# Performance work log

Hardware: AMD Instinct MI355X
Metric: run time of the kernel (lower is better)

## Reference

```python
import jax, jax.numpy as jnp
import numpy as np

GROUPS = 32
EPS = 1e-5


def group_norm(x, weight, bias):
    # x: [B, C, H, W]; normalize per (group, H, W) as torch nn.GroupNorm
    B, C, H, W = x.shape
    xg = x.reshape(B, GROUPS, C // GROUPS, H, W)
    mean = xg.mean(axis=(2, 3, 4), keepdims=True)
    var = xg.var(axis=(2, 3, 4), keepdims=True)
    xg = (xg - mean) * jax.lax.rsqrt(var + EPS)
    x = xg.reshape(B, C, H, W)
    return x * weight[None, :, None, None] + bias[None, :, None, None]


def setup_inputs() -> dict:
    key = jax.random.key(0)
    ks = jax.random.split(key, 8)
    B, C, H, W = 2, 512, 64, 64
    s = 1.0 / np.sqrt(C)  # linear-init-like scale to keep logits sane
    return {
        "x": jax.random.normal(ks[0], (B, C, H, W), dtype=jnp.float32),
        "gn_weight": jnp.ones((C,), jnp.float32),
        "gn_bias": jnp.zeros((C,), jnp.float32),
        "wq": jax.random.normal(ks[1], (C, C), jnp.float32) * s,
        "bq": jnp.zeros((C,), jnp.float32),
        "wk": jax.random.normal(ks[2], (C, C), jnp.float32) * s,
        "bk": jnp.zeros((C,), jnp.float32),
        "wv": jax.random.normal(ks[3], (C, C), jnp.float32) * s,
        "bv": jnp.zeros((C,), jnp.float32),
        "wo": jax.random.normal(ks[4], (C, C), jnp.float32) * s,
        "bo": jnp.zeros((C,), jnp.float32),
    }


def reference(x, gn_weight, gn_bias, wq, bq, wk, bk, wv, bv, wo, bo):
    B, C, H, W = x.shape
    residual = x
    h = group_norm(x, gn_weight, gn_bias)
    # [B, N, C] tokens, N = H*W
    t = h.reshape(B, C, H * W).transpose(0, 2, 1)
    q = t @ wq.T + bq
    k = t @ wk.T + bk
    v = t @ wv.T + bv
    scale = C ** (-0.5)
    # naive full attention: [B, N, N]
    attn = jax.nn.softmax(jnp.einsum("bnc,bmc->bnm", q, k) * scale, axis=-1)
    out = jnp.einsum("bnm,bmc->bnc", attn, v)
    out = out @ wo.T + bo
    out = out.transpose(0, 2, 1).reshape(B, C, H, W)
    return out + residual
```

## Files before the change

kernel.cpp:

```cpp
#include <hip/hip_runtime.h>
#include <cstddef>
#include <cstdint>


typedef __attribute__((ext_vector_type(8))) short frag8;
typedef __attribute__((ext_vector_type(4))) float f32x4;

#define GLOAD16(g, l)                                                        \
    __builtin_amdgcn_global_load_lds(                                        \
        (const __attribute__((address_space(1))) void*)(g),                  \
        (__attribute__((address_space(3))) void*)(l), 16, 0, 0)

__device__ __forceinline__ float b2f(unsigned short u) {
    union { unsigned u32; float f; } v; v.u32 = ((unsigned)u) << 16; return v.f;
}
__device__ __forceinline__ unsigned short f2bu(float f) {
    unsigned u = __float_as_uint(f);
    unsigned r = u + 0x7fffu + ((u >> 16) & 1u);
    return (unsigned short)(r >> 16);
}

__global__ __launch_bounds__(256) void cast_f32_bf16(const float* __restrict__ src,
                                                     unsigned short* __restrict__ dst,
                                                     int n) {
    int i = (blockIdx.x * 256 + threadIdx.x) * 8;
    if (i >= n) return;
    float4 a = *reinterpret_cast<const float4*>(src + i);
    float4 b = *reinterpret_cast<const float4*>(src + i + 4);
    float vv[8] = {a.x, a.y, a.z, a.w, b.x, b.y, b.z, b.w};
    union { unsigned short u16[8]; uint4 v; } o;
#pragma unroll
    for (int j = 0; j < 8; ++j) o.u16[j] = f2bu(vv[j]);
    *reinterpret_cast<uint4*>(dst + i) = o.v;
}

__global__ __launch_bounds__(256) void gn_stats(const float* __restrict__ x,
                                                float* __restrict__ stats) {
    const int tid = threadIdx.x;
    const float* p = x + (size_t)blockIdx.x * 65536;
    float s = 0.f, ss = 0.f;
    for (int i = tid * 8; i < 65536; i += 2048) {
        float4 a = *reinterpret_cast<const float4*>(p + i);
        float4 b = *reinterpret_cast<const float4*>(p + i + 4);
        float vv[8] = {a.x, a.y, a.z, a.w, b.x, b.y, b.z, b.w};
#pragma unroll
        for (int j = 0; j < 8; ++j) { s += vv[j]; ss += vv[j] * vv[j]; }
    }
#pragma unroll
    for (int o = 32; o; o >>= 1) { s += __shfl_xor(s, o, 64); ss += __shfl_xor(ss, o, 64); }
    __shared__ float rs[4], rss[4];
    int wv = tid >> 6, lane = tid & 63;
    if (lane == 0) { rs[wv] = s; rss[wv] = ss; }
    __syncthreads();
    if (tid == 0) {
        float S1 = rs[0] + rs[1] + rs[2] + rs[3];
        float S2 = rss[0] + rss[1] + rss[2] + rss[3];
        float mean = S1 * (1.f / 65536.f);
        float var  = fmaxf(S2 * (1.f / 65536.f) - mean * mean, 0.f);
        stats[blockIdx.x * 2 + 0] = mean;
        stats[blockIdx.x * 2 + 1] = rsqrtf(var + 1e-5f);
    }
}

__global__ __launch_bounds__(256) void prep_all(const float* __restrict__ x,
                                                float* __restrict__ stats,
                                                const float* __restrict__ wq,
                                                const float* __restrict__ wk,
                                                const float* __restrict__ wv,
                                                const float* __restrict__ wo,
                                                const float* __restrict__ bq,
                                                const float* __restrict__ bk,
                                                const float* __restrict__ bv,
                                                const float* __restrict__ bo,
                                                unsigned short* __restrict__ wB0,
                                                unsigned short* __restrict__ wB3,
                                                unsigned short* __restrict__ bB0,
                                                unsigned short* __restrict__ bB3) {
    const int tid = threadIdx.x;
    const int bx = blockIdx.x;
    if (bx < 64) {
        const float* p = x + (size_t)bx * 65536;
        float s = 0.f, ss = 0.f;
        for (int i = tid * 8; i < 65536; i += 2048) {
            float4 a = *reinterpret_cast<const float4*>(p + i);
            float4 b = *reinterpret_cast<const float4*>(p + i + 4);
            float vv[8] = {a.x, a.y, a.z, a.w, b.x, b.y, b.z, b.w};
#pragma unroll
            for (int j = 0; j < 8; ++j) { s += vv[j]; ss += vv[j] * vv[j]; }
        }
#pragma unroll
        for (int o = 32; o; o >>= 1) { s += __shfl_xor(s, o, 64); ss += __shfl_xor(ss, o, 64); }
        __shared__ float rs[4], rss[4];
        int wvi = tid >> 6, lane = tid & 63;
        if (lane == 0) { rs[wvi] = s; rss[wvi] = ss; }
        __syncthreads();
        if (tid == 0) {
            float S1 = rs[0] + rs[1] + rs[2] + rs[3];
            float S2 = rss[0] + rss[1] + rss[2] + rss[3];
            float mean = S1 * (1.f / 65536.f);
            float var  = fmaxf(S2 * (1.f / 65536.f) - mean * mean, 0.f);
            stats[bx * 2 + 0] = mean;
            stats[bx * 2 + 1] = rsqrtf(var + 1e-5f);
        }
    } else if (bx < 576) {
        const int j = bx - 64;
        const int w = j >> 7;
        const int b128 = j & 127;
        const float* src = (w == 0) ? wq : (w == 1) ? wk : (w == 2) ? wv : wo;
        unsigned short* dst = (w == 0) ? wB0 : (w == 1) ? wB0 + 262144
                              : (w == 2) ? wB0 + 524288 : wB3;
        int i = (b128 * 256 + tid) * 8;
        float4 a = *reinterpret_cast<const float4*>(src + i);
        float4 b = *reinterpret_cast<const float4*>(src + i + 4);
        float vv[8] = {a.x, a.y, a.z, a.w, b.x, b.y, b.z, b.w};
        union { unsigned short u16[8]; uint4 v; } o;
#pragma unroll
        for (int jj = 0; jj < 8; ++jj) o.u16[jj] = f2bu(vv[jj]);
        *reinterpret_cast<uint4*>(dst + i) = o.v;
    } else {
        const int j = bx - 576;
        const float* src = (j == 0) ? bq : (j == 1) ? bk : (j == 2) ? bv : bo;
        unsigned short* dst = (j == 0) ? bB0 : (j == 1) ? bB0 + 512
                              : (j == 2) ? bB0 + 1024 : bB3;
        int i = tid * 8;
        if (i < 512) {
            float4 a = *reinterpret_cast<const float4*>(src + i);
            float4 b = *reinterpret_cast<const float4*>(src + i + 4);
            float vv[8] = {a.x, a.y, a.z, a.w, b.x, b.y, b.z, b.w};
            union { unsigned short u16[8]; uint4 v; } o;
#pragma unroll
            for (int jj = 0; jj < 8; ++jj) o.u16[jj] = f2bu(vv[jj]);
            *reinterpret_cast<uint4*>(dst + i) = o.v;
        }
    }
}

__global__ __launch_bounds__(256) void build_t(const float* __restrict__ x,
                                               const float* __restrict__ stats,
                                               const float* __restrict__ gnw,
                                               const float* __restrict__ gnb,
                                               unsigned short* __restrict__ t) {
    __shared__ unsigned short tile[64 * 66];
    const int b = blockIdx.z, c0 = blockIdx.y * 64, hw0 = blockIdx.x * 64;
#pragma unroll
    for (int it = 0; it < 2; ++it) {
        int idx = it * 256 + threadIdx.x;
        int c = idx >> 3, v8 = idx & 7;
        int cg = c0 + c;
        int g = cg >> 4;
        float mean = stats[(b * 32 + g) * 2 + 0];
        float rstd = stats[(b * 32 + g) * 2 + 1];
        float sc = rstd * gnw[cg];
        float sh = gnb[cg] - mean * sc;
        const float* src = x + ((size_t)(b * 512 + cg)) * 4096 + hw0 + v8 * 8;
        float4 a = *reinterpret_cast<const float4*>(src);
        float4 bb = *reinterpret_cast<const float4*>(src + 4);
        float vv[8] = {a.x, a.y, a.z, a.w, bb.x, bb.y, bb.z, bb.w};
#pragma unroll
        for (int j = 0; j < 8; ++j)
            tile[c * 66 + v8 * 8 + j] = f2bu(vv[j] * sc + sh);
    }
    __syncthreads();
#pragma unroll
    for (int it = 0; it < 2; ++it) {
        int idx = it * 256 + threadIdx.x;
        int hw = idx >> 3, v8 = idx & 7;
        union { unsigned short u16[8]; uint4 v; } outv;
#pragma unroll
        for (int j = 0; j < 8; ++j) outv.u16[j] = tile[(v8 * 8 + j) * 66 + hw];
        *reinterpret_cast<uint4*>(t + ((size_t)(b * 4096 + hw0 + hw)) * 512 + c0 + v8 * 8) =
            outv.v;
    }
}

template <int MODE>
__global__ __launch_bounds__(256) void gemm_bt(const unsigned short* __restrict__ A,
                                               const unsigned short* __restrict__ B,
                                               const unsigned short* __restrict__ bias,
                                               const float* __restrict__ resid,
                                               unsigned short* __restrict__ C,
                                               float* __restrict__ Cf,
                                               int M, int N, int K, float alpha,
                                               size_t zA, size_t zB, size_t zC) {
    __shared__ __attribute__((aligned(16))) unsigned short As[128 * 32];
    __shared__ __attribute__((aligned(16))) unsigned short Bs[128 * 32];

    A += (size_t)blockIdx.z * zA;
    B += (size_t)blockIdx.z * zB;
    C += (size_t)blockIdx.z * zC;

    const int tid = threadIdx.x;
    const int lane = tid & 63, wv = tid >> 6;
    const int lrow = lane & 15, quad = lane >> 4;
    const int wr = (wv & 1) * 64, wc = (wv >> 1) * 64;

    const unsigned short* Ag = A + ((size_t)blockIdx.x * 128 + wv * 16 + (lane >> 2)) * K + (lane & 3) * 8;
    const unsigned short* Bg = B + ((size_t)blockIdx.y * 128 + wv * 16 + (lane >> 2)) * K + (lane & 3) * 8;
    unsigned short* Asw = As + wv * 512;
    unsigned short* Bsw = Bs + wv * 512;
    const size_t rowskip = (size_t)64 * K;

    f32x4 acc[4][4] = {};

    for (int k0 = 0; k0 < K; k0 += 32) {
        GLOAD16(Ag + k0,           Asw);
        GLOAD16(Ag + k0 + rowskip, Asw + 2048);
        GLOAD16(Bg + k0,           Bsw);
        GLOAD16(Bg + k0 + rowskip, Bsw + 2048);
        __syncthreads();

        frag8 af[4], bf[4];
        const unsigned short* ap = As + (wr + lrow) * 32 + quad * 8;
        const unsigned short* bp = Bs + (wc + lrow) * 32 + quad * 8;
#pragma unroll
        for (int i = 0; i < 4; ++i) af[i] = *reinterpret_cast<const frag8*>(ap + i * 512);
#pragma unroll
        for (int j = 0; j < 4; ++j) bf[j] = *reinterpret_cast<const frag8*>(bp + j * 512);
#pragma unroll
        for (int i = 0; i < 4; ++i)
#pragma unroll
            for (int j = 0; j < 4; ++j)
                acc[i][j] = __builtin_amdgcn_mfma_f32_16x16x32_bf16(af[i], bf[j], acc[i][j], 0, 0, 0);
        __syncthreads();
    }

    const int rowBase = blockIdx.x * 128 + wr + quad * 4;
    const int colBase = blockIdx.y * 128 + wc + lrow;
#pragma unroll
    for (int j = 0; j < 4; ++j) {
        const int col = colBase + j * 16;
        float badd = 0.f;
        if (MODE == 3 && bias) badd = b2f(bias[col]);
#pragma unroll
        for (int i = 0; i < 4; ++i) {
            const int row = rowBase + i * 16;
#pragma unroll
            for (int r = 0; r < 4; ++r) {
                const int rr = row + r;
                float v = acc[i][j][r];
                if (MODE == 2) v *= alpha;
                v += badd;
                if (MODE == 2) {
                    C[(size_t)rr * N + col] = f2bu(v);
                } else {
                    size_t addr = ((size_t)(rr >> 12) * 512 + col) * 4096 + (rr & 4095);
                    Cf[addr] = v + resid[addr];
                }
            }
        }
    }
}

__global__ __launch_bounds__(256) void gemm_qkv(const unsigned short* __restrict__ A,
                                                const unsigned short* __restrict__ Ball,
                                                const unsigned short* __restrict__ biasAll,
                                                unsigned short* __restrict__ q,
                                                unsigned short* __restrict__ k,
                                                unsigned short* __restrict__ vT) {
    __shared__ __attribute__((aligned(16))) unsigned short As[128 * 32];
    __shared__ __attribute__((aligned(16))) unsigned short Bs[128 * 32];
    const int K = 512;

    const int tid = threadIdx.x;
    const int lane = tid & 63, wv = tid >> 6;
    const int lrow = lane & 15, quad = lane >> 4;
    const int wr = (wv & 1) * 64, wc = (wv >> 1) * 64;

    const unsigned short* B = Ball + (size_t)blockIdx.y * 128 * 512;
    const unsigned short* Ag = A + ((size_t)blockIdx.x * 128 + wv * 16 + (lane >> 2)) * K + (lane & 3) * 8;
    const unsigned short* Bg = B + ((size_t)(wv * 16 + (lane >> 2))) * K + (lane & 3) * 8;
    unsigned short* Asw = As + wv * 512;
    unsigned short* Bsw = Bs + wv * 512;
    const size_t rowskip = (size_t)64 * K;

    f32x4 acc[4][4] = {};

    for (int k0 = 0; k0 < K; k0 += 32) {
        GLOAD16(Ag + k0,           Asw);
        GLOAD16(Ag + k0 + rowskip, Asw + 2048);
        GLOAD16(Bg + k0,           Bsw);
        GLOAD16(Bg + k0 + rowskip, Bsw + 2048);
        __syncthreads();

        frag8 af[4], bf[4];
        const unsigned short* ap = As + (wr + lrow) * 32 + quad * 8;
        const unsigned short* bp = Bs + (wc + lrow) * 32 + quad * 8;
#pragma unroll
        for (int i = 0; i < 4; ++i) af[i] = *reinterpret_cast<const frag8*>(ap + i * 512);
#pragma unroll
        for (int j = 0; j < 4; ++j) bf[j] = *reinterpret_cast<const frag8*>(bp + j * 512);
#pragma unroll
        for (int i = 0; i < 4; ++i)
#pragma unroll
            for (int j = 0; j < 4; ++j)
                acc[i][j] = __builtin_amdgcn_mfma_f32_16x16x32_bf16(af[i], bf[j], acc[i][j], 0, 0, 0);
        __syncthreads();
    }

    const int rowBase = blockIdx.x * 128 + wr + quad * 4;
    const int colBase = wc + lrow;
    const int gbase = blockIdx.y * 128;
#pragma unroll
    for (int j = 0; j < 4; ++j) {
        const int colL = colBase + j * 16;
        const int gcol = gbase + colL;
        const float badd = b2f(biasAll[gcol]);
#pragma unroll
        for (int i = 0; i < 4; ++i) {
            const int row = rowBase + i * 16;
#pragma unroll
            for (int r = 0; r < 4; ++r) {
                const int rr = row + r;
                float v = acc[i][j][r] + badd;
                if (blockIdx.y < 4) {
                    q[(size_t)rr * 512 + gcol] = f2bu(v);
                } else if (blockIdx.y < 8) {
                    k[(size_t)rr * 512 + (gcol - 512)] = f2bu(v);
                } else {
                    int ch = gcol - 1024;
                    vT[((size_t)(rr >> 12) * 512 + ch) * 4096 + (rr & 4095)] = f2bu(v);
                }
            }
        }
    }
}

__global__ __launch_bounds__(512, 4) void s_gemm(const unsigned short* __restrict__ qIn,
                                                 const unsigned short* __restrict__ kIn,
                                                 unsigned short* __restrict__ Sout,
                                                 float alpha) {
    __shared__ __attribute__((aligned(16))) unsigned short Ab[2][8192];
    __shared__ __attribute__((aligned(16))) unsigned short Bb[2][8192];

    const int tid = threadIdx.x;
    const int lane = tid & 63, w = tid >> 6;
    const int lrow = lane & 15, quad = lane >> 4;
    const int wm = w & 1, wn = w >> 1;
    const int z = blockIdx.z;

    const unsigned short* A = qIn + (size_t)z * 2097152;
    const unsigned short* B = kIn + (size_t)z * 2097152;
    unsigned short* C = Sout + (size_t)z * 16777216;

    const int srow = w * 8 + (lane >> 3);
    const int skc  = ((lane & 7) ^ (lane >> 3)) * 8;
    const unsigned short* Ag = A + ((size_t)blockIdx.x * 128 + srow) * 512 + skc;
    const unsigned short* Bg = B + ((size_t)blockIdx.y * 128 + srow) * 512 + skc;
    const size_t rowskip64 = (size_t)64 * 512;

    f32x4 acc[4][2] = {};

#define SG_STAGE(cur, kt)                                                    \
    do {                                                                     \
        const unsigned short* a_ = Ag + (size_t)(kt) * 64;                   \
        const unsigned short* b_ = Bg + (size_t)(kt) * 64;                   \
        GLOAD16(a_,             &Ab[cur][w * 512]);                          \
        GLOAD16(a_ + rowskip64, &Ab[cur][4096 + w * 512]);                   \
        GLOAD16(b_,             &Bb[cur][w * 512]);                          \
        GLOAD16(b_ + rowskip64, &Bb[cur][4096 + w * 512]);                   \
    } while (0)

#define SG_COMPUTE(cur)                                                      \
    do {                                                                     \
        const int rbA = (wm * 64 + lrow) * 64;                               \
        const int rbB = (wn * 32 + lrow) * 64;                               \
        _Pragma("unroll")                                                    \
        for (int kk = 0; kk < 2; ++kk) {                                     \
            const int us = (((kk * 4 + quad) ^ (lrow & 7)) * 8);             \
            frag8 af[4], bf[2];                                              \
            _Pragma("unroll")                                                \
            for (int i = 0; i < 4; ++i)                                      \
                af[i] = *reinterpret_cast<const frag8*>(&Ab[cur][rbA + i * 1024 + us]); \
            _Pragma("unroll")                                                \
            for (int j2 = 0; j2 < 2; ++j2)                                   \
                bf[j2] = *reinterpret_cast<const frag8*>(&Bb[cur][rbB + j2 * 1024 + us]); \
            _Pragma("unroll")                                                \
            for (int i = 0; i < 4; ++i)                                      \
                _Pragma("unroll")                                            \
                for (int j2 = 0; j2 < 2; ++j2)                               \
                    acc[i][j2] = __builtin_amdgcn_mfma_f32_16x16x32_bf16(    \
                        af[i], bf[j2], acc[i][j2], 0, 0, 0);                 \
        }                                                                    \
    } while (0)

    SG_STAGE(0, 0);
    asm volatile("s_waitcnt vmcnt(0)" ::: "memory");
    __builtin_amdgcn_s_barrier();
    __builtin_amdgcn_sched_barrier(0);

    int cur = 0;
    for (int kt = 0; kt < 7; ++kt) {
        SG_STAGE(cur ^ 1, kt + 1);
        __builtin_amdgcn_sched_barrier(0);
        SG_COMPUTE(cur);
        asm volatile("s_waitcnt vmcnt(0)" ::: "memory");
        __builtin_amdgcn_s_barrier();
        __builtin_amdgcn_sched_barrier(0);
        cur ^= 1;
    }
    SG_COMPUTE(cur);

#undef SG_STAGE
#undef SG_COMPUTE

    const int rowBase = blockIdx.x * 128 + wm * 64 + quad * 4;
    const int colBase = blockIdx.y * 128 + wn * 32 + lrow;
#pragma unroll
    for (int j2 = 0; j2 < 2; ++j2) {
        const int col = colBase + j2 * 16;
#pragma unroll
        for (int i = 0; i < 4; ++i) {
            const int row = rowBase + i * 16;
#pragma unroll
            for (int r = 0; r < 4; ++r)
                C[(size_t)(row + r) * 4096 + col] = f2bu(acc[i][j2][r] * alpha);
        }
    }
}

__global__ __launch_bounds__(512, 6) void pv_gemm(const unsigned short* __restrict__ S0,
                                                  const unsigned short* __restrict__ vT0,
                                                  unsigned short* __restrict__ O0) {
    __shared__ __attribute__((aligned(16))) unsigned short Ab[2][4096];
    __shared__ __attribute__((aligned(16))) unsigned short Bb[2][8192];

    const int tid = threadIdx.x;
    const int lane = tid & 63, w = tid >> 6;
    const int lrow = lane & 15, quad = lane >> 4;
    const int wm = w & 1, wn = w >> 1;

    const int id = blockIdx.x;
    const int g  = id & 7;
    const int yt = g & 3, z = g >> 2;
    const int xt = id >> 3;

    const unsigned short* A = S0 + (size_t)z * 16777216;
    const unsigned short* B = vT0 + (size_t)z * 2097152;
    unsigned short* C = O0 + (size_t)z * 2097152;

    const int srow = w * 8 + (lane >> 3);
    const int skc  = ((lane & 7) ^ (lane >> 3)) * 8;
    const unsigned short* Ag = A + ((size_t)xt * 64 + srow) * 4096 + skc;
    const unsigned short* Bg = B + ((size_t)(yt * 128 + srow)) * 4096 + skc;
    const size_t rowskip64 = (size_t)64 * 4096;

    f32x4 acc[2][2] = {};

#define PV_STAGE(cur, kt)                                                    \
    do {                                                                     \
        const unsigned short* a_ = Ag + (size_t)(kt) * 64;                   \
        const unsigned short* b_ = Bg + (size_t)(kt) * 64;                   \
        GLOAD16(a_,             &Ab[cur][w * 512]);                          \
        GLOAD16(b_,             &Bb[cur][w * 512]);                          \
        GLOAD16(b_ + rowskip64, &Bb[cur][4096 + w * 512]);                   \
    } while (0)

#define PV_COMPUTE(cur)                                                      \
    do {                                                                     \
        const int rbA = (wm * 32 + lrow) * 64;                               \
        const int rbB = (wn * 32 + lrow) * 64;                               \
        _Pragma("unroll")                                                    \
        for (int kk = 0; kk < 2; ++kk) {                                     \
            const int us = (((kk * 4 + quad) ^ (lrow & 7)) * 8);             \
            frag8 af[2], bf[2];                                              \
            _Pragma("unroll")                                                \
            for (int i = 0; i < 2; ++i)                                      \
                af[i] = *reinterpret_cast<const frag8*>(&Ab[cur][rbA + i * 1024 + us]); \
            _Pragma("unroll")                                                \
            for (int j2 = 0; j2 < 2; ++j2)                                   \
                bf[j2] = *reinterpret_cast<const frag8*>(&Bb[cur][rbB + j2 * 1024 + us]); \
            _Pragma("unroll")                                                \
            for (int i = 0; i < 2; ++i)                                      \
                _Pragma("unroll")                                            \
                for (int j2 = 0; j2 < 2; ++j2)                               \
                    acc[i][j2] = __builtin_amdgcn_mfma_f32_16x16x32_bf16(    \
                        af[i], bf[j2], acc[i][j2], 0, 0, 0);                 \
        }                                                                    \
    } while (0)

    PV_STAGE(0, 0);
    asm volatile("s_waitcnt vmcnt(0)" ::: "memory");
    __builtin_amdgcn_s_barrier();
    __builtin_amdgcn_sched_barrier(0);

    int cur = 0;
    for (int kt = 0; kt < 63; ++kt) {
        PV_STAGE(cur ^ 1, kt + 1);
        __builtin_amdgcn_sched_barrier(0);
        PV_COMPUTE(cur);
        asm volatile("s_waitcnt vmcnt(0)" ::: "memory");
        __builtin_amdgcn_s_barrier();
        __builtin_amdgcn_sched_barrier(0);
        cur ^= 1;
    }
    PV_COMPUTE(cur);

#undef PV_STAGE
#undef PV_COMPUTE

    const int rowBase = xt * 64 + wm * 32 + quad * 4;
    const int colBase = yt * 128 + wn * 32 + lrow;
#pragma unroll
    for (int j2 = 0; j2 < 2; ++j2) {
        const int col = colBase + j2 * 16;
#pragma unroll
        for (int i = 0; i < 2; ++i) {
            const int row = rowBase + i * 16;
#pragma unroll
            for (int r = 0; r < 4; ++r)
                C[(size_t)(row + r) * 512 + col] = f2bu(acc[i][j2][r]);
        }
    }
}

__global__ __launch_bounds__(512, 2) void ksplit_o(const unsigned short* __restrict__ A,
                                                   const unsigned short* __restrict__ B,
                                                   unsigned short* __restrict__ C,
                                                   int N, int K) {
    __shared__ __attribute__((aligned(16))) unsigned char smem[65536];
    const int tid = threadIdx.x;
    const int lane = tid & 63, wv = tid >> 6;
    const int lrow = lane & 15, quad = lane >> 4;
    const int colhalf = wv & 1;
    const int kz = wv >> 1;
    const int Kw = K >> 2;
    const int yt = blockIdx.x;
    const int xt = blockIdx.y;

    unsigned short* Aw = (unsigned short*)smem + wv * 4096;
    unsigned short* Bw = Aw + 2048;

    const unsigned short* Ag = A + ((size_t)xt * 64 + (lane >> 2)) * K + kz * Kw + (lane & 3) * 8;
    const unsigned short* Bg = B + ((size_t)(yt * 128 + colhalf * 64 + (lane >> 2))) * K + kz * Kw + (lane & 3) * 8;
    const size_t rowskip16 = (size_t)16 * K;

    f32x4 acc[4][4] = {};

    for (int k0 = 0; k0 < Kw; k0 += 32) {
        uint4 av[4], bv_[4];
#pragma unroll
        for (int i = 0; i < 4; ++i) {
            av[i]  = *reinterpret_cast<const uint4*>(Ag + k0 + i * rowskip16);
            bv_[i] = *reinterpret_cast<const uint4*>(Bg + k0 + i * rowskip16);
        }
#pragma unroll
        for (int i = 0; i < 4; ++i) {
            *reinterpret_cast<uint4*>(Aw + i * 512 + lane * 8) = av[i];
            *reinterpret_cast<uint4*>(Bw + i * 512 + lane * 8) = bv_[i];
        }
        frag8 af[4], bf[4];
#pragma unroll
        for (int i = 0; i < 4; ++i) {
            af[i] = *reinterpret_cast<const frag8*>(Aw + i * 512 + lrow * 32 + quad * 8);
            bf[i] = *reinterpret_cast<const frag8*>(Bw + i * 512 + lrow * 32 + quad * 8);
        }
        __builtin_amdgcn_s_setprio(1);
#pragma unroll
        for (int i = 0; i < 4; ++i)
#pragma unroll
            for (int j = 0; j < 4; ++j)
                acc[i][j] = __builtin_amdgcn_mfma_f32_16x16x32_bf16(af[i], bf[j], acc[i][j], 0, 0, 0);
        __builtin_amdgcn_s_setprio(0);
    }

    __syncthreads();
    float* fbase = (float*)smem;
    if (kz == 0 || kz == 2) {
        float* f = fbase + (colhalf * 2 + (kz >> 1)) * 4096;
#pragma unroll
        for (int i = 0; i < 4; ++i)
#pragma unroll
            for (int j = 0; j < 4; ++j)
#pragma unroll
                for (int r = 0; r < 4; ++r)
                    f[(i * 16 + quad * 4 + r) * 64 + j * 16 + lrow] = acc[i][j][r];
    }
    __syncthreads();
    if (kz == 1 || kz == 3) {
        float* f = fbase + (colhalf * 2 + (kz >> 1)) * 4096;
#pragma unroll
        for (int i = 0; i < 4; ++i)
#pragma unroll
            for (int j = 0; j < 4; ++j)
#pragma unroll
                for (int r = 0; r < 4; ++r)
                    f[(i * 16 + quad * 4 + r) * 64 + j * 16 + lrow] += acc[i][j][r];
    }
    __syncthreads();
#pragma unroll
    for (int e = 0; e < 16; ++e) {
        int idx = e * 512 + tid;
        int row = idx >> 7, colL = idx & 127;
        int ch = colL >> 6, c = colL & 63;
        float v = fbase[(ch * 2 + 0) * 4096 + row * 64 + c] +
                  fbase[(ch * 2 + 1) * 4096 + row * 64 + c];
        C[((size_t)xt * 64 + row) * N + yt * 128 + colL] = f2bu(v);
    }
}

__global__ __launch_bounds__(256) void softmax_rows(unsigned short* __restrict__ S) {
    __shared__ float red[8];
    const int tid = threadIdx.x;
    const int wv = tid >> 6, lane = tid & 63;
    unsigned short* p = S + (size_t)blockIdx.x * 4096 + tid * 16;

    uint4 r0 = *reinterpret_cast<const uint4*>(p);
    uint4 r1 = *reinterpret_cast<const uint4*>(p + 8);
    unsigned w[8] = {r0.x, r0.y, r0.z, r0.w, r1.x, r1.y, r1.z, r1.w};
    float v[16];
#pragma unroll
    for (int q2 = 0; q2 < 8; ++q2) {
        v[q2 * 2 + 0] = b2f((unsigned short)(w[q2] & 0xffffu));
        v[q2 * 2 + 1] = b2f((unsigned short)(w[q2] >> 16));
    }
    float m = -3.0e38f;
#pragma unroll
    for (int q2 = 0; q2 < 16; ++q2) m = fmaxf(m, v[q2]);
#pragma unroll
    for (int o = 32; o; o >>= 1) m = fmaxf(m, __shfl_xor(m, o, 64));
    if (lane == 0) red[wv] = m;
    __syncthreads();
    m = fmaxf(fmaxf(red[0], red[1]), fmaxf(red[2], red[3]));

    float s = 0.f;
#pragma unroll
    for (int q2 = 0; q2 < 16; ++q2) { v[q2] = __expf(v[q2] - m); s += v[q2]; }
#pragma unroll
    for (int o = 32; o; o >>= 1) s += __shfl_xor(s, o, 64);
    if (lane == 0) red[4 + wv] = s;
    __syncthreads();
    s = red[4] + red[5] + red[6] + red[7];
    const float inv = 1.f / s;

    unsigned ow[8];
#pragma unroll
    for (int q2 = 0; q2 < 8; ++q2) {
        unsigned lo = f2bu(v[q2 * 2 + 0] * inv);
        unsigned hi = f2bu(v[q2 * 2 + 1] * inv);
        ow[q2] = lo | (hi << 16);
    }
    uint4 o0 = {ow[0], ow[1], ow[2], ow[3]};
    uint4 o1 = {ow[4], ow[5], ow[6], ow[7]};
    *reinterpret_cast<uint4*>(p) = o0;
    *reinterpret_cast<uint4*>(p + 8) = o1;
}

__global__ void write_sentinel_f32(float* out, float code) {
    if (threadIdx.x == 0) out[0] = code;
}

extern "C" void kernel_launch(void* const* d_in, const int* in_sizes, int n_in,
                              void* d_out, int out_size, void* d_ws, size_t ws_size,
                              hipStream_t stream) {
    const float* x   = (const float*)d_in[0];
    const float* gnw = (const float*)d_in[1];
    const float* gnb = (const float*)d_in[2];
    const float* wq  = (const float*)d_in[3];
    const float* bq  = (const float*)d_in[4];
    const float* wk  = (const float*)d_in[5];
    const float* bk  = (const float*)d_in[6];
    const float* wv  = (const float*)d_in[7];
    const float* bv  = (const float*)d_in[8];
    const float* wo  = (const float*)d_in[9];
    const float* bo  = (const float*)d_in[10];
    float* out = (float*)d_out;

    bool shapes_ok = (n_in == 11 && in_sizes[0] == 4194304 && in_sizes[1] == 512 &&
                      in_sizes[3] == 262144 && out_size == 4194304);
    size_t half = ws_size / 2;
    if (!shapes_ok || half < (size_t)17831936 + 128 * 4096) {
        write_sentinel_f32<<<1, 64, 0, stream>>>(out, shapes_ok ? 8000.f : 9000.f);
        return;
    }

    unsigned short* ws = (unsigned short*)d_ws;
    unsigned short* t  = ws;
    unsigned short* q  = ws + 4194304;
    unsigned short* k  = ws + 8388608;
    unsigned short* vT = ws + 12582912;
    unsigned short* o  = t;
    const float scale = 0.044194173824159216f;

    unsigned short* wB0 = ws + 16777216;
    unsigned short* bB0 = ws + 17825792;
    float* stats = (float*)(ws + 17827840);

    if (half >= (size_t)50594816) {
        unsigned short* S   = ws + 16777216;
        unsigned short* wB3 = ws + 50331648;
        unsigned short* bB3 = ws + 50593792;
        prep_all<<<580, 256, 0, stream>>>(x, stats, wq, wk, wv, wo, bq, bk, bv, bo,
                                          wB0, wB3, bB0, bB3);
        build_t<<<dim3(64, 8, 2), 256, 0, stream>>>(x, stats, gnw, gnb, t);
        gemm_qkv<<<dim3(64, 12), 256, 0, stream>>>(t, wB0, bB0, q, k, vT);
        s_gemm<<<dim3(32, 32, 2), 512, 0, stream>>>(q, k, S, scale);
        softmax_rows<<<8192, 256, 0, stream>>>(S);
        pv_gemm<<<512, 512, 0, stream>>>(S, vT, o);
        gemm_bt<3><<<dim3(64, 4), 256, 0, stream>>>(o, wB3, bB3, x, nullptr, out,
                                                    8192, 512, 512, 1.f, 0, 0, 0);
        return;
    }

    unsigned short* wB3 = ws + 17563648;
    unsigned short* bB3 = ws + 17827328;

    cast_f32_bf16<<<128, 256, 0, stream>>>(wq, wB0,          262144);
    cast_f32_bf16<<<128, 256, 0, stream>>>(wk, wB0 + 262144, 262144);
    cast_f32_bf16<<<128, 256, 0, stream>>>(wv, wB0 + 524288, 262144);
    cast_f32_bf16<<<1, 256, 0, stream>>>(bq, bB0,        512);
    cast_f32_bf16<<<1, 256, 0, stream>>>(bk, bB0 + 512,  512);
    cast_f32_bf16<<<1, 256, 0, stream>>>(bv, bB0 + 1024, 512);

    gn_stats<<<64, 256, 0, stream>>>(x, stats);
    build_t<<<dim3(64, 8, 2), 256, 0, stream>>>(x, stats, gnw, gnb, t);
    gemm_qkv<<<dim3(64, 12), 256, 0, stream>>>(t, wB0, bB0, q, k, vT);

    if (half >= (size_t)50331648) {
        unsigned short* S = ws + 16777216;
        s_gemm<<<dim3(32, 32, 2), 512, 0, stream>>>(q, k, S, scale);
        softmax_rows<<<8192, 256, 0, stream>>>(S);
        pv_gemm<<<512, 512, 0, stream>>>(S, vT, o);
    } else if (half >= (size_t)33554432) {
        unsigned short* S = ws + 16777216;
        for (int b = 0; b < 2; ++b) {
            const unsigned short* qb  = q  + (size_t)b * 2097152;
            const unsigned short* kb  = k  + (size_t)b * 2097152;
            const unsigned short* vTb = vT + (size_t)b * 2097152;
            unsigned short*       ob  = o  + (size_t)b * 2097152;
            gemm_bt<2><<<dim3(32, 32), 256, 0, stream>>>(qb, kb, nullptr, nullptr, S, nullptr,
                                                         4096, 4096, 512, scale, 0, 0, 0);
            softmax_rows<<<4096, 256, 0, stream>>>(S);
            ksplit_o<<<dim3(4, 64), 512, 0, stream>>>(S, vTb, ob, 512, 4096);
        }
    } else {
        unsigned short* S = ws + 17831936;
        size_t avail = half - 17831936;
        int R = 4096;
        while (R > 128 && (size_t)R * 4096 > avail) R >>= 1;
        for (int b = 0; b < 2; ++b) {
            const unsigned short* qb  = q  + (size_t)b * 2097152;
            const unsigned short* kb  = k  + (size_t)b * 2097152;
            const unsigned short* vTb = vT + (size_t)b * 2097152;
            unsigned short*       ob  = o  + (size_t)b * 2097152;
            for (int r0 = 0; r0 < 4096; r0 += R) {
                gemm_bt<2><<<dim3(R / 128, 32), 256, 0, stream>>>(
                    qb + (size_t)r0 * 512, kb, nullptr, nullptr, S, nullptr, R, 4096, 512, scale,
                    0, 0, 0);
                softmax_rows<<<R, 256, 0, stream>>>(S);
                ksplit_o<<<dim3(4, R / 64), 512, 0, stream>>>(
                    S, vTb, ob + (size_t)r0 * 512, 512, 4096);
            }
        }
    }
    cast_f32_bf16<<<128, 256, 0, stream>>>(wo, wB3, 262144);
    cast_f32_bf16<<<1, 256, 0, stream>>>(bo, bB3, 512);
    gemm_bt<3><<<dim3(64, 4), 256, 0, stream>>>(o, wB3, bB3, x, nullptr, out,
                                                8192, 512, 512, 1.f, 0, 0, 0);
}
```

Measured before the change: 264.5 us.

## Fuse softmax normalization into PV GEMM using precomputed row max and sum

Replaces the in-place softmax pass with a kernel that only computes each row's max and inverse sum of exponentials. The PV GEMM then exponentiates and normalizes the score fragments as it loads them. This removes the write-back of the full score matrix. In exchange, the exponentials are recomputed in every column tile of the GEMM, adding VALU work to its inner loop, and the path needs a slightly larger workspace.

Measured after the change: 347.3 us. 31.3% more time.

```diff
diff --git a/kernel.cpp b/kernel.cpp
--- a/kernel.cpp
+++ b/kernel.cpp
@@ -418,9 +418,50 @@
     }
 }
 
+__global__ __launch_bounds__(256) void row_stats(const unsigned short* __restrict__ S,
+                                                 float* __restrict__ rstat) {
+    __shared__ float red[8];
+    const int tid = threadIdx.x;
+    const int wv = tid >> 6, lane = tid & 63;
+    const unsigned short* p = S + (size_t)blockIdx.x * 4096 + tid * 16;
+
+    uint4 r0 = *reinterpret_cast<const uint4*>(p);
+    uint4 r1 = *reinterpret_cast<const uint4*>(p + 8);
+    unsigned w[8] = {r0.x, r0.y, r0.z, r0.w, r1.x, r1.y, r1.z, r1.w};
+    float v[16];
+#pragma unroll
+    for (int q2 = 0; q2 < 8; ++q2) {
+        v[q2 * 2 + 0] = b2f((unsigned short)(w[q2] & 0xffffu));
+        v[q2 * 2 + 1] = b2f((unsigned short)(w[q2] >> 16));
+    }
+    float m = -3.0e38f;
+#pragma unroll
+    for (int q2 = 0; q2 < 16; ++q2) m = fmaxf(m, v[q2]);
+#pragma unroll
+    for (int o = 32; o; o >>= 1) m = fmaxf(m, __shfl_xor(m, o, 64));
+    if (lane == 0) red[wv] = m;
+    __syncthreads();
+    m = fmaxf(fmaxf(red[0], red[1]), fmaxf(red[2], red[3]));
+
+    float s = 0.f;
+#pragma unroll
+    for (int q2 = 0; q2 < 16; ++q2) s += __expf(v[q2] - m);
+#pragma unroll
+    for (int o = 32; o; o >>= 1) s += __shfl_xor(s, o, 64);
+    if (lane == 0) red[4 + wv] = s;
+    __syncthreads();
+    if (tid == 0) {
+        s = red[4] + red[5] + red[6] + red[7];
+        rstat[blockIdx.x * 2 + 0] = m;
+        rstat[blockIdx.x * 2 + 1] = 1.f / s;
+    }
+}
+
+template <int FUSED>
 __global__ __launch_bounds__(512, 6) void pv_gemm(const unsigned short* __restrict__ S0,
                                                   const unsigned short* __restrict__ vT0,
-                                                  unsigned short* __restrict__ O0) {
+                                                  unsigned short* __restrict__ O0,
+                                                  const float* __restrict__ rstat) {
     __shared__ __attribute__((aligned(16))) unsigned short Ab[2][4096];
     __shared__ __attribute__((aligned(16))) unsigned short Bb[2][8192];
 
@@ -437,6 +478,15 @@
     const unsigned short* A = S0 + (size_t)z * 16777216;
     const unsigned short* B = vT0 + (size_t)z * 2097152;
     unsigned short* C = O0 + (size_t)z * 2097152;
+
+    float mrow[2] = {0.f, 0.f}, irow[2] = {1.f, 1.f};
+    if (FUSED) {
+        const int grow = z * 4096 + xt * 64 + wm * 32 + lrow;
+        mrow[0] = rstat[(size_t)grow * 2 + 0];
+        irow[0] = rstat[(size_t)grow * 2 + 1];
+        mrow[1] = rstat[(size_t)(grow + 16) * 2 + 0];
+        irow[1] = rstat[(size_t)(grow + 16) * 2 + 1];
+    }
 
     const int srow = w * 8 + (lane >> 3);
     const int skc  = ((lane & 7) ^ (lane >> 3)) * 8;
@@ -466,6 +516,18 @@
             _Pragma("unroll")                                                \
             for (int i = 0; i < 2; ++i)                                      \
                 af[i] = *reinterpret_cast<const frag8*>(&Ab[cur][rbA + i * 1024 + us]); \
+            if (FUSED) {                                                     \
+                _Pragma("unroll")                                            \
+                for (int i = 0; i < 2; ++i) {                                \
+                    frag8 a = af[i], r;                                      \
+                    _Pragma("unroll")                                        \
+                    for (int e = 0; e < 8; ++e) {                            \
+                        float f = b2f((unsigned short)a[e]);                 \
+                        r[e] = (short)f2bu(__expf(f - mrow[i]) * irow[i]);   \
+                    }                                                        \
+                    af[i] = r;                                               \
+                }                                                            \
+            }                                                                \
             _Pragma("unroll")                                                \
             for (int j2 = 0; j2 < 2; ++j2)                                   \
                 bf[j2] = *reinterpret_cast<const frag8*>(&Bb[cur][rbB + j2 * 1024 + us]); \
@@ -685,6 +747,23 @@
     unsigned short* bB0 = ws + 17825792;
     float* stats = (float*)(ws + 17827840);
 
+    if (half >= (size_t)50627584) {
+        unsigned short* S   = ws + 16777216;
+        unsigned short* wB3 = ws + 50331648;
+        unsigned short* bB3 = ws + 50593792;
+        float* rstat = (float*)(ws + 50594816);
+        prep_all<<<580, 256, 0, stream>>>(x, stats, wq, wk, wv, wo, bq, bk, bv, bo,
+                                          wB0, wB3, bB0, bB3);
+        build_t<<<dim3(64, 8, 2), 256, 0, stream>>>(x, stats, gnw, gnb, t);
+        gemm_qkv<<<dim3(64, 12), 256, 0, stream>>>(t, wB0, bB0, q, k, vT);
+        s_gemm<<<dim3(32, 32, 2), 512, 0, stream>>>(q, k, S, scale);
+        row_stats<<<8192, 256, 0, stream>>>(S, rstat);
+        pv_gemm<1><<<512, 512, 0, stream>>>(S, vT, o, rstat);
+        gemm_bt<3><<<dim3(64, 4), 256, 0, stream>>>(o, wB3, bB3, x, nullptr, out,
+                                                    8192, 512, 512, 1.f, 0, 0, 0);
+        return;
+    }
+
     if (half >= (size_t)50594816) {
         unsigned short* S   = ws + 16777216;
         unsigned short* wB3 = ws + 50331648;
@@ -695,7 +774,7 @@
         gemm_qkv<<<dim3(64, 12), 256, 0, stream>>>(t, wB0, bB0, q, k, vT);
         s_gemm<<<dim3(32, 32, 2), 512, 0, stream>>>(q, k, S, scale);
         softmax_rows<<<8192, 256, 0, stream>>>(S);
-        pv_gemm<<<512, 512, 0, stream>>>(S, vT, o);
+        pv_gemm<0><<<512, 512, 0, stream>>>(S, vT, o, nullptr);
         gemm_bt<3><<<dim3(64, 4), 256, 0, stream>>>(o, wB3, bB3, x, nullptr, out,
                                                     8192, 512, 512, 1.f, 0, 0, 0);
         return;
@@ -719,7 +798,7 @@
         unsigned short* S = ws + 16777216;
         s_gemm<<<dim3(32, 32, 2), 512, 0, stream>>>(q, k, S, scale);
         softmax_rows<<<8192, 256, 0, stream>>>(S);
-        pv_gemm<<<512, 512, 0, stream>>>(S, vT, o);
+        pv_gemm<0><<<512, 512, 0, stream>>>(S, vT, o, nullptr);
     } else if (half >= (size_t)33554432) {
         unsigned short* S = ws + 16777216;
         for (int b = 0; b < 2; ++b) {
```
